# Kernel tuning notes

Hardware: AMD Instinct MI355X
Metric: run time of the kernel (lower is better)

## Reference

```python
import jax, jax.numpy as jnp
import numpy as np
import math

D_MODEL = 1024
N_HEADS = 16
HEAD_DIM = D_MODEL // N_HEADS  # 64
KV_DIM = 4 * HEAD_DIM          # 256
THETA = 10000.0
B, T = 2, 2048


def setup_inputs() -> dict:
    key = jax.random.key(0)
    ks = jax.random.split(key, 14)
    s = lambda k, *sh: jax.random.normal(k, sh, dtype=jnp.float32) * 0.02
    inp = {
        "x": jax.random.normal(ks[0], (B, T, D_MODEL), dtype=jnp.float32),
        "mask": jnp.tril(jnp.ones((T, T), dtype=jnp.int32))[None, None],  # causal [1,1,T,T]
        "Wq": s(ks[1], D_MODEL, D_MODEL), "bq": jnp.zeros((D_MODEL,), jnp.float32),
        "Wkv": s(ks[2], D_MODEL, KV_DIM), "bkv": jnp.zeros((KV_DIM,), jnp.float32),
        "Wk": s(ks[3], KV_DIM, D_MODEL), "bk": jnp.zeros((D_MODEL,), jnp.float32),
        "Wv": s(ks[4], KV_DIM, D_MODEL), "bv": jnp.zeros((D_MODEL,), jnp.float32),
        "Wo": s(ks[5], D_MODEL, D_MODEL), "bo": jnp.zeros((D_MODEL,), jnp.float32),
        "Wkr": s(ks[6], HEAD_DIM, HEAD_DIM),  # decoupled k_rope linear, no bias
    }
    return inp


def _rotate_half(x):
    x1, x2 = jnp.split(x, 2, axis=-1)
    return jnp.concatenate((-x2, x1), axis=-1)


def reference(x, mask, Wq, bq, Wkv, bkv, Wk, bk, Wv, bv, Wo, bo, Wkr):
    Bq, Tq, C = x.shape
    kv = x @ Wkv + bkv                                # [B,T,KV_DIM]
    k = (kv @ Wk + bk).reshape(Bq, Tq, N_HEADS, HEAD_DIM).transpose(0, 2, 1, 3)
    v = (kv @ Wv + bv).reshape(Bq, Tq, N_HEADS, HEAD_DIM).transpose(0, 2, 1, 3)
    q = (x @ Wq + bq).reshape(Bq, Tq, N_HEADS, HEAD_DIM).transpose(0, 2, 1, 3)

    # standard RoPE on q
    inv_freq = 1.0 / (THETA ** (jnp.arange(0, HEAD_DIM, 2, dtype=jnp.float32) / HEAD_DIM))
    t = jnp.arange(Tq, dtype=jnp.float32)
    freqs = t[:, None] * inv_freq[None, :]            # [T, D/2]
    emb = jnp.concatenate((freqs, freqs), axis=-1)    # [T, D]
    q = q * jnp.cos(emb) + _rotate_half(q) * jnp.sin(emb)

    # decoupled position path for k: scale by position index, then linear
    k = (k * t[None, None, :, None]) @ Wkr            # [B,H,T,D]

    attn = jnp.einsum('bhtd,bhsd->bhts', q, k) * (1.0 / math.sqrt(HEAD_DIM))
    attn = jnp.where(mask == 0, -jnp.inf, attn)
    attn = jax.nn.softmax(attn, axis=-1)
    y = jnp.einsum('bhts,bhsd->bhtd', attn, v)
    y = y.transpose(0, 2, 1, 3).reshape(Bq, Tq, C)
    return y @ Wo + bo
```

## Files before the change

### kernel.cpp

```cpp
#include <hip/hip_runtime.h>
#include <hip/hip_bf16.h>
#include <math.h>

typedef __bf16 bf16x8 __attribute__((ext_vector_type(8)));
typedef __bf16 bf16x4 __attribute__((ext_vector_type(4)));
typedef float  f32x4  __attribute__((ext_vector_type(4)));

#define T_SEQ 2048
#define NH    16
#define HD    64
#define DM    1024
#define QSCALE 0.18033688011112043f

__device__ __forceinline__ f32x4 mfma16(bf16x8 a, bf16x8 b, f32x4 c) {
    return __builtin_amdgcn_mfma_f32_16x16x32_bf16(a, b, c, 0, 0, 0);
}

__device__ __forceinline__ void gl2lds(const void* g, void* l) {
    __builtin_amdgcn_global_load_lds(
        (const __attribute__((address_space(1))) void*)g,
        (__attribute__((address_space(3))) void*)l, 16, 0, 0);
}

__device__ __forceinline__ void tsplit_body(const float* __restrict__ in,
                                            __bf16* __restrict__ oh, __bf16* __restrict__ ol,
                                            int K, int N, int n0, int k0, int SPLIT,
                                            float* tile )
{
    const int tid = threadIdx.x;
#pragma unroll
    for (int it = 0; it < 2; ++it) {
        int r = it * 32 + (tid >> 3), c8 = (tid & 7) * 8;
        f32x4 a0 = *(const f32x4*)&in[(size_t)(k0 + r) * N + n0 + c8];
        f32x4 a1 = *(const f32x4*)&in[(size_t)(k0 + r) * N + n0 + c8 + 4];
#pragma unroll
        for (int j = 0; j < 4; ++j) { tile[r * 65 + c8 + j] = a0[j]; tile[r * 65 + c8 + 4 + j] = a1[j]; }
    }
    __syncthreads();
    const int n = tid >> 2, kb = (tid & 3) * 16;
    bf16x8 h0, h1, l0, l1;
#pragma unroll
    for (int j = 0; j < 8; ++j) {
        float v0 = tile[(kb + j) * 65 + n], v1 = tile[(kb + 8 + j) * 65 + n];
        __bf16 hb0 = (__bf16)v0, hb1 = (__bf16)v1;
        h0[j] = hb0; h1[j] = hb1;
        if (SPLIT) { l0[j] = (__bf16)(v0 - (float)hb0); l1[j] = (__bf16)(v1 - (float)hb1); }
    }
    size_t o = (size_t)(n0 + n) * K + k0 + kb;
    *(bf16x8*)&oh[o] = h0; *(bf16x8*)&oh[o + 8] = h1;
    if (SPLIT) { *(bf16x8*)&ol[o] = l0; *(bf16x8*)&ol[o + 8] = l1; }
}

__global__ __launch_bounds__(256)
void prep(const float* __restrict__ x, const float* __restrict__ Wq,
          const float* __restrict__ Wkv, const float* __restrict__ Wv,
          const float* __restrict__ Wo, const float* __restrict__ Wk,
          const float* __restrict__ Wkr, const float* __restrict__ bk,
          __bf16* xh, __bf16* xl, __bf16* Wqt_h, __bf16* Wqt_l,
          __bf16* Wkvt_h, __bf16* Wkvt_l, __bf16* Wvt, __bf16* Wot,
          __bf16* W2th, __bf16* W2tl, float* b2)
{
    __shared__ float tile[64 * 65];
    const int g = blockIdx.x, tid = threadIdx.x;
    if (g < 2048) {
        size_t idx = ((size_t)g * 256 + tid) * 8;
        f32x4 a0 = *(const f32x4*)&x[idx];
        f32x4 a1 = *(const f32x4*)&x[idx + 4];
        bf16x8 h, l;
#pragma unroll
        for (int j = 0; j < 4; ++j) {
            __bf16 h0 = (__bf16)a0[j];
            h[j]     = h0; l[j]     = (__bf16)(a0[j] - (float)h0);
            __bf16 h1 = (__bf16)a1[j];
            h[4 + j] = h1; l[4 + j] = (__bf16)(a1[j] - (float)h1);
        }
        *(bf16x8*)&xh[idx] = h;
        *(bf16x8*)&xl[idx] = l;
    } else if (g < 2304) {
        int i = g - 2048;
        tsplit_body(Wq, Wqt_h, Wqt_l, 1024, 1024, (i & 15) * 64, (i >> 4) * 64, 1, tile);
    } else if (g < 2368) {
        int i = g - 2304;
        tsplit_body(Wkv, Wkvt_h, Wkvt_l, 1024, 256, (i & 3) * 64, (i >> 2) * 64, 1, tile);
    } else if (g < 2432) {
        int i = g - 2368;
        tsplit_body(Wv, Wvt, nullptr, 256, 1024, (i & 15) * 64, (i >> 4) * 64, 0, tile);
    } else if (g < 2688) {
        int i = g - 2432;
        tsplit_body(Wo, Wot, nullptr, 1024, 1024, (i & 15) * 64, (i >> 4) * 64, 0, tile);
    } else {
        int o    = (g - 2688) * 256 + tid;
        int rowk = o >> 10, col = o & 1023;
        int h = col >> 6, d = col & 63;
        float acc = 0.0f;
        if (rowk < 256) {
#pragma unroll 8
            for (int j = 0; j < 64; ++j)
                acc += Wk[(size_t)rowk * DM + h * HD + j] * Wkr[j * HD + d];
            __bf16 hb = (__bf16)acc;
            W2th[(size_t)col * 256 + rowk] = hb;
            W2tl[(size_t)col * 256 + rowk] = (__bf16)(acc - (float)hb);
        } else {
#pragma unroll 8
            for (int j = 0; j < 64; ++j)
                acc += bk[h * HD + j] * Wkr[j * HD + d];
            b2[col] = acc;
        }
    }
}

template <int DUALA, int DUALB, int OUTM, int EPI>
__device__ __forceinline__
void gemm_body(char* smem,
               const __bf16* __restrict__ Ahi, const __bf16* __restrict__ Alo,
               const __bf16* __restrict__ Bhi, const __bf16* __restrict__ Blo,
               const float* __restrict__ bias, void* __restrict__ Cp,
               void* __restrict__ Cp2, int m0, int n0, int N, int K)
{
    const int tid  = threadIdx.x;
    const int w    = tid >> 6;
    const int lane = tid & 63;
    const int l16  = lane & 15;
    const int quad = lane >> 4;
    const int wy   = w >> 1, wx = w & 1;

    f32x4 acc[4][4];
#pragma unroll
    for (int i = 0; i < 4; ++i)
#pragma unroll
        for (int j = 0; j < 4; ++j) acc[i][j] = (f32x4)0.0f;

    auto stage = [&](int k0, int buf) {
        char* bb = smem + buf * 32768;
#pragma unroll
        for (int i = 0; i < 2; ++i) {
            int s = i * 256 + tid, row = s >> 2, c8 = (s & 3) * 8;
            size_t aoff = (size_t)(m0 + row) * K + k0 + c8;
            size_t boff = (size_t)(n0 + row) * K + k0 + c8;
            char*  dst  = bb + (row * 32 + c8) * 2;
            gl2lds(&Ahi[aoff], dst);
            if (DUALA) gl2lds(&Alo[aoff], dst + 8192);
            gl2lds(&Bhi[boff], dst + 16384);
            if (DUALB) gl2lds(&Blo[boff], dst + 24576);
        }
    };

    stage(0, 0);
    const int J = K >> 5;
    for (int j = 0; j < J; ++j) {
        __syncthreads();
        if (j + 1 < J) stage((j + 1) << 5, (j + 1) & 1);

        const __bf16* Ah = (const __bf16*)(smem + (j & 1) * 32768);
        const __bf16* Al = Ah + 4096;
        const __bf16* Bh = Ah + 8192;
        const __bf16* Bl = Ah + 12288;

        bf16x8 bfh[4], bfl[4];
#pragma unroll
        for (int ct = 0; ct < 4; ++ct) {
            bfh[ct] = *(const bf16x8*)&Bh[(wx * 64 + ct * 16 + l16) * 32 + quad * 8];
            if (DUALB) bfl[ct] = *(const bf16x8*)&Bl[(wx * 64 + ct * 16 + l16) * 32 + quad * 8];
        }
#pragma unroll
        for (int mf = 0; mf < 4; ++mf) {
            bf16x8 ah = *(const bf16x8*)&Ah[(wy * 64 + mf * 16 + l16) * 32 + quad * 8];
            bf16x8 al;
            if (DUALA) al = *(const bf16x8*)&Al[(wy * 64 + mf * 16 + l16) * 32 + quad * 8];
#pragma unroll
            for (int ct = 0; ct < 4; ++ct) {
                acc[mf][ct] = mfma16(ah, bfh[ct], acc[mf][ct]);
                if (DUALA) acc[mf][ct] = mfma16(al, bfh[ct], acc[mf][ct]);
                if (DUALB) acc[mf][ct] = mfma16(ah, bfl[ct], acc[mf][ct]);
            }
        }
    }

    float bias_v[4];
#pragma unroll
    for (int ct = 0; ct < 4; ++ct)
        bias_v[ct] = bias ? bias[n0 + wx * 64 + ct * 16 + l16] : 0.0f;

    if (EPI == 1) {
        __bf16* Chi = (__bf16*)Cp;
        __bf16* Clo = (__bf16*)Cp2;
#pragma unroll
        for (int mf = 0; mf < 4; ++mf) {
#pragma unroll
            for (int r = 0; r < 4; ++r) {
                int   m = m0 + wy * 64 + mf * 16 + quad * 4 + r;
                float t = (float)(m & (T_SEQ - 1));
#pragma unroll
                for (int ct = 0; ct < 2; ++ct) {
                    int   d   = ct * 16 + l16;
                    float inv = powf(10000.0f, -(float)d * (1.0f / 32.0f));
                    float sv, cv;
                    sincosf(t * inv, &sv, &cv);
                    float lo = acc[mf][ct][r]     + bias_v[ct];
                    float hi = acc[mf][ct + 2][r] + bias_v[ct + 2];
                    float v0 = (lo * cv - hi * sv) * QSCALE;
                    float v1 = (hi * cv + lo * sv) * QSCALE;
                    size_t i0 = (size_t)m * N + n0 + wx * 64 + d;
                    size_t i1 = i0 + 32;
                    __bf16 h0 = (__bf16)v0, h1 = (__bf16)v1;
                    Chi[i0] = h0; Clo[i0] = (__bf16)(v0 - (float)h0);
                    Chi[i1] = h1; Clo[i1] = (__bf16)(v1 - (float)h1);
                }
            }
        }
    } else if (EPI == 3) {
        __syncthreads();
        __bf16* vt = (__bf16*)(smem + w * 9216);
#pragma unroll
        for (int mf = 0; mf < 4; ++mf)
#pragma unroll
            for (int ct = 0; ct < 4; ++ct)
#pragma unroll
                for (int r = 0; r < 4; ++r)
                    vt[(ct * 16 + l16) * 72 + mf * 16 + quad * 4 + r] =
                        (__bf16)(acc[mf][ct][r] + bias_v[ct]);
        const int bb   = m0 >> 11;
        const int head = (n0 + wx * 64) >> 6;
        const int bh   = bb * 16 + head;
        __bf16* out    = (__bf16*)Cp;
        size_t  gbase  = ((size_t)(bh * 64 + lane)) * T_SEQ + (m0 & (T_SEQ - 1)) + wy * 64;
#pragma unroll
        for (int j8 = 0; j8 < 8; ++j8)
            *(bf16x8*)&out[gbase + j8 * 8] = *(const bf16x8*)&vt[lane * 72 + j8 * 8];
    } else {
#pragma unroll
        for (int mf = 0; mf < 4; ++mf) {
#pragma unroll
            for (int r = 0; r < 4; ++r) {
                int   m     = m0 + wy * 64 + mf * 16 + quad * 4 + r;
                float scale = (EPI == 2) ? (float)(m & (T_SEQ - 1)) : 1.0f;
#pragma unroll
                for (int ct = 0; ct < 4; ++ct) {
                    float  v   = (acc[mf][ct][r] + bias_v[ct]) * scale;
                    size_t idx = (size_t)m * N + n0 + wx * 64 + ct * 16 + l16;
                    if (OUTM == 1)      ((float*)Cp)[idx]  = v;
                    else if (OUTM == 0) ((__bf16*)Cp)[idx] = (__bf16)v;
                    else {
                        __bf16 hb = (__bf16)v;
                        ((__bf16*)Cp)[idx]  = hb;
                        ((__bf16*)Cp2)[idx] = (__bf16)(v - (float)hb);
                    }
                }
            }
        }
    }
}

__global__ __launch_bounds__(256)
void gemm_qkv(const __bf16* xh, const __bf16* xl,
              const __bf16* Wqt_h, const __bf16* Wqt_l, const float* bq,
              __bf16* qhi, __bf16* qlo,
              const __bf16* Wkvt_h, const __bf16* Wkvt_l, const float* bkv,
              __bf16* kvhi, __bf16* kvlo)
{
    __shared__ __attribute__((aligned(16))) char smem[65536];
    const int m0 = blockIdx.y * 128;
    if (blockIdx.x < 2)
        gemm_body<1, 1, 2, 0>(smem, xh, xl, Wkvt_h, Wkvt_l, bkv, kvhi, kvlo,
                              m0, blockIdx.x * 128, 256, 1024);
    else
        gemm_body<1, 1, 2, 1>(smem, xh, xl, Wqt_h, Wqt_l, bq, qhi, qlo,
                              m0, (blockIdx.x - 2) * 128, 1024, 1024);
}

__global__ __launch_bounds__(256)
void gemm_kv2(const __bf16* kvhi, const __bf16* kvlo,
              const __bf16* W2th, const __bf16* W2tl, const float* b2,
              __bf16* khi, __bf16* klo,
              const __bf16* Wvt, const float* bv, __bf16* vtg)
{
    __shared__ __attribute__((aligned(16))) char smem[65536];
    const int m0 = blockIdx.y * 128;
    if (blockIdx.x < 8)
        gemm_body<1, 1, 2, 2>(smem, kvhi, kvlo, W2th, W2tl, b2, khi, klo,
                              m0, blockIdx.x * 128, 1024, 256);
    else
        gemm_body<1, 0, 0, 3>(smem, kvhi, kvlo, Wvt, Wvt, bv, vtg, nullptr,
                              m0, (blockIdx.x - 8) * 128, 1024, 256);
}

__global__ __launch_bounds__(256)
void gemm_o(const __bf16* ybb, const __bf16* Wot, const float* bo, float* out)
{
    __shared__ __attribute__((aligned(16))) char smem[65536];
    gemm_body<0, 0, 1, 0>(smem, ybb, ybb, Wot, Wot, bo, out, nullptr,
                          blockIdx.y * 128, blockIdx.x * 128, 1024, 1024);
}

#define KSP 72
#define PSP 72
__global__ __launch_bounds__(256, 2)
void attn_v7(const __bf16* __restrict__ qhi, const __bf16* __restrict__ qlo,
             const __bf16* __restrict__ khi, const __bf16* __restrict__ klo,
             const __bf16* __restrict__ vtg, __bf16* __restrict__ yb)
{
    __shared__ __attribute__((aligned(16))) __bf16 Kh2[2][64 * KSP];
    __shared__ __attribute__((aligned(16))) __bf16 Kl2[2][64 * KSP];
    __shared__ __attribute__((aligned(16))) __bf16 Vt2[2][64 * KSP];
    __shared__ __attribute__((aligned(16))) __bf16 Pw[4][16 * PSP];

    const int tid  = threadIdx.x;
    const int w    = tid >> 6;
    const int lane = tid & 63;
    const int l16  = lane & 15;
    const int quad = lane >> 4;

    const int g  = blockIdx.x;
    const int bh = g & 31, a = g >> 5;
    const int b  = bh >> 4, h = bh & 15;

    const int srow = tid >> 3, sc8 = (tid & 7) * 8;

    for (int ph = 0; ph < 2; ++ph) {
        const int u  = ph ? a : (31 - a);
        const int q0 = u * 64;

        bf16x8 qh[2], ql[2];
        {
            const int    qr   = q0 + 16 * w + l16;
            const size_t qoff = (size_t)(b * T_SEQ + qr) * DM + h * HD;
#pragma unroll
            for (int s = 0; s < 2; ++s) {
                qh[s] = *(const bf16x8*)&qhi[qoff + s * 32 + quad * 8];
                ql[s] = *(const bf16x8*)&qlo[qoff + s * 32 + quad * 8];
            }
        }

        f32x4 o[4];
#pragma unroll
        for (int i = 0; i < 4; ++i) o[i] = (f32x4)0.0f;
        float m_i = -1e30f, l_i = 0.f;

        bf16x8 kr[2], lr[2], vr[2];
#pragma unroll
        for (int it = 0; it < 2; ++it) {
            int    r  = it * 32 + srow;
            size_t gk = (size_t)(b * T_SEQ + r) * DM + h * HD + sc8;
            kr[it] = *(const bf16x8*)&khi[gk];
            lr[it] = *(const bf16x8*)&klo[gk];
            vr[it] = *(const bf16x8*)&vtg[(size_t)(bh * HD + r) * T_SEQ + sc8];
        }
        __syncthreads();
#pragma unroll
        for (int it = 0; it < 2; ++it) {
            int r = it * 32 + srow;
            *(bf16x8*)&Kh2[0][r * KSP + sc8] = kr[it];
            *(bf16x8*)&Kl2[0][r * KSP + sc8] = lr[it];
            *(bf16x8*)&Vt2[0][r * KSP + sc8] = vr[it];
        }

        for (int j0 = 0; j0 <= q0; j0 += 64) {
            const int  cur = (j0 >> 6) & 1;
            const bool pre = (j0 + 64 <= q0);
            __syncthreads();

            if (pre) {
#pragma unroll
                for (int it = 0; it < 2; ++it) {
                    int    r  = it * 32 + srow;
                    size_t gk = (size_t)(b * T_SEQ + j0 + 64 + r) * DM + h * HD + sc8;
                    kr[it] = *(const bf16x8*)&khi[gk];
                    lr[it] = *(const bf16x8*)&klo[gk];
                    vr[it] = *(const bf16x8*)&vtg[(size_t)(bh * HD + r) * T_SEQ + j0 + 64 + sc8];
                }
            }

            const __bf16* Kh = Kh2[cur];
            const __bf16* Kl = Kl2[cur];
            const __bf16* Vt = Vt2[cur];

            f32x4 sa[4];
#pragma unroll
            for (int i = 0; i < 4; ++i) sa[i] = (f32x4)0.0f;
#pragma unroll
            for (int s = 0; s < 2; ++s) {
#pragma unroll
                for (int kc = 0; kc < 4; ++kc) {
                    bf16x8 kh = *(const bf16x8*)&Kh[(kc * 16 + l16) * KSP + s * 32 + quad * 8];
                    bf16x8 kv = *(const bf16x8*)&Kl[(kc * 16 + l16) * KSP + s * 32 + quad * 8];
                    sa[kc] = mfma16(kh, qh[s], sa[kc]);
                    sa[kc] = mfma16(kv, qh[s], sa[kc]);
                    sa[kc] = mfma16(kh, ql[s], sa[kc]);
                }
            }

            const int  qr   = q0 + 16 * w + l16;
            const bool need = (j0 + 63 > q0 + 16 * w);
            if (need) {
#pragma unroll
                for (int kc = 0; kc < 4; ++kc)
#pragma unroll
                    for (int r = 0; r < 4; ++r)
                        if (j0 + kc * 16 + quad * 4 + r > qr) sa[kc][r] = -1e30f;
            }
            float mx = -1e30f;
#pragma unroll
            for (int kc = 0; kc < 4; ++kc)
#pragma unroll
                for (int r = 0; r < 4; ++r) mx = fmaxf(mx, sa[kc][r]);
            mx = fmaxf(mx, __shfl_xor(mx, 16));
            mx = fmaxf(mx, __shfl_xor(mx, 32));
            float mn    = fmaxf(fmaxf(m_i, mx), -1e20f);
            float alpha = exp2f(m_i - mn);
            m_i = mn;
            float rs = 0.f;
            __bf16* pw = &Pw[w][0];
#pragma unroll
            for (int kc = 0; kc < 4; ++kc) {
                float p0 = exp2f(sa[kc][0] - mn);
                float p1 = exp2f(sa[kc][1] - mn);
                float p2 = exp2f(sa[kc][2] - mn);
                float p3 = exp2f(sa[kc][3] - mn);
                rs += (p0 + p1) + (p2 + p3);
                bf16x4 pk = { (__bf16)p0, (__bf16)p1, (__bf16)p2, (__bf16)p3 };
                *(bf16x4*)&pw[l16 * PSP + kc * 16 + quad * 4] = pk;
            }
            rs += __shfl_xor(rs, 16);
            rs += __shfl_xor(rs, 32);
            l_i = l_i * alpha + rs;
#pragma unroll
            for (int dc = 0; dc < 4; ++dc) o[dc] *= alpha;

#pragma unroll
            for (int s = 0; s < 2; ++s) {
                bf16x8 pb = *(const bf16x8*)&pw[l16 * PSP + s * 32 + quad * 8];
#pragma unroll
                for (int dc = 0; dc < 4; ++dc) {
                    bf16x8 va = *(const bf16x8*)&Vt[(dc * 16 + l16) * KSP + s * 32 + quad * 8];
                    o[dc] = mfma16(va, pb, o[dc]);
                }
            }

            if (pre) {
                __bf16* nKh = Kh2[cur ^ 1];
                __bf16* nKl = Kl2[cur ^ 1];
                __bf16* nVt = Vt2[cur ^ 1];
#pragma unroll
                for (int it = 0; it < 2; ++it) {
                    int r = it * 32 + srow;
                    *(bf16x8*)&nKh[r * KSP + sc8] = kr[it];
                    *(bf16x8*)&nKl[r * KSP + sc8] = lr[it];
                    *(bf16x8*)&nVt[r * KSP + sc8] = vr[it];
                }
            }
        }

        {
            float   invl = 1.0f / l_i;
            __bf16* pw   = &Pw[w][0];
#pragma unroll
            for (int dc = 0; dc < 4; ++dc) {
                bf16x4 ov = { (__bf16)(o[dc][0] * invl), (__bf16)(o[dc][1] * invl),
                              (__bf16)(o[dc][2] * invl), (__bf16)(o[dc][3] * invl) };
                *(bf16x4*)&pw[l16 * PSP + dc * 16 + quad * 4] = ov;
            }
            const int qrl  = lane >> 2;
            const int dch  = (lane & 3) * 16;
            const int qrow = q0 + 16 * w + qrl;
            const __bf16* src = &pw[qrl * PSP + dch];
            __bf16*       dst = &yb[(size_t)(b * T_SEQ + qrow) * DM + h * HD + dch];
            *(bf16x8*)dst       = *(const bf16x8*)src;
            *(bf16x8*)(dst + 8) = *(const bf16x8*)(src + 8);
        }
    }
}

extern "C" void kernel_launch(void* const* d_in, const int* in_sizes, int n_in,
                              void* d_out, int out_size, void* d_ws, size_t ws_size,
                              hipStream_t stream)
{
    (void)in_sizes; (void)n_in; (void)out_size; (void)ws_size;

    const float* x   = (const float*)d_in[0];
    const float* Wq  = (const float*)d_in[2];
    const float* bq  = (const float*)d_in[3];
    const float* Wkv = (const float*)d_in[4];
    const float* bkv = (const float*)d_in[5];
    const float* Wk  = (const float*)d_in[6];
    const float* bk  = (const float*)d_in[7];
    const float* Wv  = (const float*)d_in[8];
    const float* bv  = (const float*)d_in[9];
    const float* Wo  = (const float*)d_in[10];
    const float* bo  = (const float*)d_in[11];
    const float* Wkr = (const float*)d_in[12];

    const int    BT = 2 * T_SEQ;
    const size_t MB = 1024 * 1024;
    char* base = (char*)d_ws;

    __bf16* xhi    = (__bf16*)(base +  0 * MB);
    __bf16* xlo    = (__bf16*)(base +  8 * MB);
    __bf16* qhi    = (__bf16*)(base + 16 * MB);
    __bf16* qlo    = (__bf16*)(base + 24 * MB);
    __bf16* Wqt_h  = (__bf16*)(base + 32 * MB);
    __bf16* Wqt_l  = (__bf16*)(base + 34 * MB);
    __bf16* Wkvt_h = (__bf16*)(base + 36 * MB);
    __bf16* Wkvt_l = (__bf16*)(base + 37 * MB);
    __bf16* kvhi   = (__bf16*)(base + 38 * MB);
    __bf16* kvlo   = (__bf16*)(base + 40 * MB);
    __bf16* W2t_h  = (__bf16*)(base + 42 * MB);
    __bf16* W2t_l  = (__bf16*)(base + 42 * MB + 512 * 1024);
    __bf16* Wvt    = (__bf16*)(base + 43 * MB);
    __bf16* Wot    = (__bf16*)(base + 43 * MB + 512 * 1024);
    float*  b2     = (float*) (base + 45 * MB + 512 * 1024);
    __bf16* vtg    = (__bf16*)(base +  8 * MB);
    __bf16* ybb    = (__bf16*)(base +  0 * MB);
    __bf16* khi    = (__bf16*)d_out;
    __bf16* klo    = (__bf16*)d_out + (size_t)BT * DM;

    dim3 blk(256);
    prep<<<3716, blk, 0, stream>>>(x, Wq, Wkv, Wv, Wo, Wk, Wkr, bk,
                                   xhi, xlo, Wqt_h, Wqt_l, Wkvt_h, Wkvt_l,
                                   Wvt, Wot, W2t_h, W2t_l, b2);
    gemm_qkv<<<dim3(10, 32), blk, 0, stream>>>(xhi, xlo, Wqt_h, Wqt_l, bq, qhi, qlo,
                                               Wkvt_h, Wkvt_l, bkv, kvhi, kvlo);
    gemm_kv2<<<dim3(16, 32), blk, 0, stream>>>(kvhi, kvlo, W2t_h, W2t_l, b2,
                                               khi, klo, Wvt, bv, vtg);
    attn_v7<<<512, blk, 0, stream>>>(qhi, qlo, khi, klo, vtg, ybb);
    gemm_o<<<dim3(8, 32), blk, 0, stream>>>(ybb, Wot, bo, (float*)d_out);
}
```

Baseline: 257.7 us.

## Load V fragments straight from global in attention; retile output GEMM to 128x64

```diff
diff --git a/kernel.cpp b/kernel.cpp
--- a/kernel.cpp
+++ b/kernel.cpp
@@ -285,30 +285,89 @@
 }
 
 __global__ __launch_bounds__(256)
-void gemm_o(const __bf16* ybb, const __bf16* Wot, const float* bo, float* out)
+void gemm_o(const __bf16* __restrict__ ybb, const __bf16* __restrict__ Wot,
+            const float* __restrict__ bo, float* __restrict__ out)
 {
     __shared__ __attribute__((aligned(16))) char smem[65536];
-    gemm_body<0, 0, 1, 0>(smem, ybb, ybb, Wot, Wot, bo, out, nullptr,
-                          blockIdx.y * 128, blockIdx.x * 128, 1024, 1024);
-}
-
-#define KSP 72
-#define PSP 72
-__global__ __launch_bounds__(256, 2)
-void attn_v7(const __bf16* __restrict__ qhi, const __bf16* __restrict__ qlo,
-             const __bf16* __restrict__ khi, const __bf16* __restrict__ klo,
-             const __bf16* __restrict__ vtg, __bf16* __restrict__ yb)
-{
-    __shared__ __attribute__((aligned(16))) __bf16 Kh2[2][64 * KSP];
-    __shared__ __attribute__((aligned(16))) __bf16 Kl2[2][64 * KSP];
-    __shared__ __attribute__((aligned(16))) __bf16 Vt2[2][64 * KSP];
-    __shared__ __attribute__((aligned(16))) __bf16 Pw[4][16 * PSP];
-
     const int tid  = threadIdx.x;
     const int w    = tid >> 6;
     const int lane = tid & 63;
     const int l16  = lane & 15;
     const int quad = lane >> 4;
+    const int m0   = blockIdx.y * 128;
+    const int n0   = blockIdx.x * 64;
+    const int K    = 1024, N = 1024;
+
+    f32x4 acc[2][4];
+#pragma unroll
+    for (int i = 0; i < 2; ++i)
+#pragma unroll
+        for (int j = 0; j < 4; ++j) acc[i][j] = (f32x4)0.0f;
+
+    auto stage = [&](int k0, int buf) {
+        char* bb = smem + buf * 32768;
+#pragma unroll
+        for (int i = 0; i < 2; ++i) {
+            int s = i * 256 + tid, row = s >> 2, c8 = (s & 3) * 8;
+            gl2lds(&ybb[(size_t)(m0 + row) * K + k0 + c8], bb + (row * 32 + c8) * 2);
+        }
+        {
+            int s = 512 + tid, br = (s >> 2) - 128, c8 = (s & 3) * 8;
+            gl2lds(&Wot[(size_t)(n0 + br) * K + k0 + c8], bb + 16384 + (br * 32 + c8) * 2);
+        }
+    };
+
+    stage(0, 0);
+    for (int j = 0; j < 32; ++j) {
+        __syncthreads();
+        if (j + 1 < 32) stage((j + 1) << 5, (j + 1) & 1);
+
+        const __bf16* Ah = (const __bf16*)(smem + (j & 1) * 32768);
+        const __bf16* Bh = Ah + 8192;
+
+        bf16x8 bfh[4];
+#pragma unroll
+        for (int ct = 0; ct < 4; ++ct)
+            bfh[ct] = *(const bf16x8*)&Bh[(ct * 16 + l16) * 32 + quad * 8];
+#pragma unroll
+        for (int mf = 0; mf < 2; ++mf) {
+            bf16x8 ah = *(const bf16x8*)&Ah[(w * 32 + mf * 16 + l16) * 32 + quad * 8];
+#pragma unroll
+            for (int ct = 0; ct < 4; ++ct)
+                acc[mf][ct] = mfma16(ah, bfh[ct], acc[mf][ct]);
+        }
+    }
+
+    float bias_v[4];
+#pragma unroll
+    for (int ct = 0; ct < 4; ++ct) bias_v[ct] = bo[n0 + ct * 16 + l16];
+#pragma unroll
+    for (int mf = 0; mf < 2; ++mf)
+#pragma unroll
+        for (int r = 0; r < 4; ++r) {
+            int m = m0 + w * 32 + mf * 16 + quad * 4 + r;
+#pragma unroll
+            for (int ct = 0; ct < 4; ++ct)
+                out[(size_t)m * N + n0 + ct * 16 + l16] = acc[mf][ct][r] + bias_v[ct];
+        }
+}
+
+#define KSP 72
+#define PSP 72
+__global__ __launch_bounds__(256, 2)
+void attn_v8(const __bf16* __restrict__ qhi, const __bf16* __restrict__ qlo,
+             const __bf16* __restrict__ khi, const __bf16* __restrict__ klo,
+             const __bf16* __restrict__ vtg, __bf16* __restrict__ yb)
+{
+    __shared__ __attribute__((aligned(16))) __bf16 Kh2[2][64 * KSP];
+    __shared__ __attribute__((aligned(16))) __bf16 Kl2[2][64 * KSP];
+    __shared__ __attribute__((aligned(16))) __bf16 Pw[4][16 * PSP];
+
+    const int tid  = threadIdx.x;
+    const int w    = tid >> 6;
+    const int lane = tid & 63;
+    const int l16  = lane & 15;
+    const int quad = lane >> 4;
 
     const int g  = blockIdx.x;
     const int bh = g & 31, a = g >> 5;
@@ -336,14 +395,13 @@
         for (int i = 0; i < 4; ++i) o[i] = (f32x4)0.0f;
         float m_i = -1e30f, l_i = 0.f;
 
-        bf16x8 kr[2], lr[2], vr[2];
+        bf16x8 kr[2], lr[2];
 #pragma unroll
         for (int it = 0; it < 2; ++it) {
             int    r  = it * 32 + srow;
             size_t gk = (size_t)(b * T_SEQ + r) * DM + h * HD + sc8;
             kr[it] = *(const bf16x8*)&khi[gk];
             lr[it] = *(const bf16x8*)&klo[gk];
-            vr[it] = *(const bf16x8*)&vtg[(size_t)(bh * HD + r) * T_SEQ + sc8];
         }
         __syncthreads();
 #pragma unroll
@@ -351,13 +409,20 @@
             int r = it * 32 + srow;
             *(bf16x8*)&Kh2[0][r * KSP + sc8] = kr[it];
             *(bf16x8*)&Kl2[0][r * KSP + sc8] = lr[it];
-            *(bf16x8*)&Vt2[0][r * KSP + sc8] = vr[it];
         }
 
         for (int j0 = 0; j0 <= q0; j0 += 64) {
             const int  cur = (j0 >> 6) & 1;
             const bool pre = (j0 + 64 <= q0);
             __syncthreads();
+
+            bf16x8 va[2][4];
+#pragma unroll
+            for (int s = 0; s < 2; ++s)
+#pragma unroll
+                for (int dc = 0; dc < 4; ++dc)
+                    va[s][dc] = *(const bf16x8*)
+                        &vtg[(size_t)(bh * HD + dc * 16 + l16) * T_SEQ + j0 + s * 32 + quad * 8];
 
             if (pre) {
 #pragma unroll
@@ -366,13 +431,11 @@
                     size_t gk = (size_t)(b * T_SEQ + j0 + 64 + r) * DM + h * HD + sc8;
                     kr[it] = *(const bf16x8*)&khi[gk];
                     lr[it] = *(const bf16x8*)&klo[gk];
-                    vr[it] = *(const bf16x8*)&vtg[(size_t)(bh * HD + r) * T_SEQ + j0 + 64 + sc8];
                 }
             }
 
             const __bf16* Kh = Kh2[cur];
             const __bf16* Kl = Kl2[cur];
-            const __bf16* Vt = Vt2[cur];
 
             f32x4 sa[4];
 #pragma unroll
@@ -430,22 +493,18 @@
             for (int s = 0; s < 2; ++s) {
                 bf16x8 pb = *(const bf16x8*)&pw[l16 * PSP + s * 32 + quad * 8];
 #pragma unroll
-                for (int dc = 0; dc < 4; ++dc) {
-                    bf16x8 va = *(const bf16x8*)&Vt[(dc * 16 + l16) * KSP + s * 32 + quad * 8];
-                    o[dc] = mfma16(va, pb, o[dc]);
-                }
+                for (int dc = 0; dc < 4; ++dc)
+                    o[dc] = mfma16(va[s][dc], pb, o[dc]);
             }
 
             if (pre) {
                 __bf16* nKh = Kh2[cur ^ 1];
                 __bf16* nKl = Kl2[cur ^ 1];
-                __bf16* nVt = Vt2[cur ^ 1];
 #pragma unroll
                 for (int it = 0; it < 2; ++it) {
                     int r = it * 32 + srow;
                     *(bf16x8*)&nKh[r * KSP + sc8] = kr[it];
                     *(bf16x8*)&nKl[r * KSP + sc8] = lr[it];
-                    *(bf16x8*)&nVt[r * KSP + sc8] = vr[it];
                 }
             }
         }
@@ -521,6 +580,6 @@
                                                Wkvt_h, Wkvt_l, bkv, kvhi, kvlo);
     gemm_kv2<<<dim3(16, 32), blk, 0, stream>>>(kvhi, kvlo, W2t_h, W2t_l, b2,
                                                khi, klo, Wvt, bv, vtg);
-    attn_v7<<<512, blk, 0, stream>>>(qhi, qlo, khi, klo, vtg, ybb);
-    gemm_o<<<dim3(8, 32), blk, 0, stream>>>(ybb, Wot, bo, (float*)d_out);
-}
+    attn_v8<<<512, blk, 0, stream>>>(qhi, qlo, khi, klo, vtg, ybb);
+    gemm_o<<<dim3(16, 32), blk, 0, stream>>>(ybb, Wot, bo, (float*)d_out);
+}
```

After: 291.1 us. +13.0%, slower.
